# Performance work log

Measured on AMD Instinct MI355X. Metric: run time of the kernel, lower is better.

Reference implementation:

```python
import jax, jax.numpy as jnp
import numpy as np
from jax.ops import segment_sum, segment_max

N, E, C, L = 50000, 600000, 128, 4
H = 2 * C  # GENConv MLP hidden = expansion(2) * in_channels
EPS_MSG = 1e-7   # GENConv message eps
EPS_LN = 1e-5    # PyG LayerNorm eps (graph mode)
EPS_GN = 1e-5    # GraphNorm eps
EPS_SM = 1e-16   # PyG softmax denominator eps


def setup_inputs() -> dict:
    key = jax.random.key(0)
    ks = jax.random.split(key, 8)
    s = 0.05
    return dict(
        x=jax.random.normal(ks[0], (N, C), jnp.float32),
        src=jax.random.randint(ks[1], (E,), 0, N),
        dst=jax.random.randint(ks[2], (E,), 0, N),
        W1=jax.random.normal(ks[3], (L, C, H), jnp.float32) * s,
        b1=jnp.zeros((L, H), jnp.float32),
        ln_w=jnp.ones((L, H), jnp.float32),
        ln_b=jnp.zeros((L, H), jnp.float32),
        W2=jax.random.normal(ks[4], (L, H, C), jnp.float32) * s,
        b2=jnp.zeros((L, C), jnp.float32),
        t=jnp.ones((L,), jnp.float32),      # learn_t=True, init t=1.0
        gn_w=jnp.ones((L, C), jnp.float32),
        gn_b=jnp.zeros((L, C), jnp.float32),
        gn_a=jnp.ones((L, C), jnp.float32),  # GraphNorm mean_scale
        lin_w=jax.random.normal(ks[5], (C, 1), jnp.float32) * s,
        lin_b=jnp.zeros((1,), jnp.float32),
    )


def graph_norm(x, w, b, a):
    # single graph: per-channel mean over nodes
    mean = x.mean(axis=0)
    out = x - a * mean
    var = (out * out).mean(axis=0)
    return w * out / jnp.sqrt(var + EPS_GN) + b


def gen_conv(x, src, dst, t, W1, b1, ln_w, ln_b, W2, b2):
    # message: relu(x_j) + eps  (no edge_attr)
    msg = jax.nn.relu(x[src]) + EPS_MSG           # [E, C]
    z = t * msg
    m = segment_max(z, dst, num_segments=N)        # [N, C]
    ex = jnp.exp(z - m[dst])
    den = segment_sum(ex, dst, num_segments=N) + EPS_SM
    alpha = ex / den[dst]                          # per-node per-channel softmax
    agg = segment_sum(msg * alpha, dst, num_segments=N)  # [N, C]
    out = agg + x                                  # root add
    # MLP([C, 2C, C]) with PyG LayerNorm (graph mode) + ReLU between layers
    h = out @ W1 + b1                              # [N, H]
    h = (h - h.mean()) / (h.std() + EPS_LN)        # graph-mode LN: scalar stats
    h = jax.nn.relu(h * ln_w + ln_b)
    return h @ W2 + b2                             # [N, C]


def reference(x, src, dst, W1, b1, ln_w, ln_b, W2, b2, t, gn_w, gn_b, gn_a, lin_w, lin_b):
    for l in range(L):
        # DeepGCNLayer block='res+': norm -> act -> (dropout=0) -> conv, residual add
        h = graph_norm(x, gn_w[l], gn_b[l], gn_a[l])
        h = jax.nn.relu(h)
        h = gen_conv(h, src, dst, t[l], W1[l], b1[l], ln_w[l], ln_b[l], W2[l], b2[l])
        x = x + h
    return x @ lin_w + lin_b                       # [N, 1]
```

## Files before the change

kernel.cpp:

```cpp
#include <hip/hip_runtime.h>

#define C_DIM 128
#define H_DIM 256
#define L_NUM 4

typedef __attribute__((ext_vector_type(8))) short bf16x8;
typedef __attribute__((ext_vector_type(4))) float f32x4;

__device__ __forceinline__ unsigned short f2bf(float f){
  unsigned u = __builtin_bit_cast(unsigned, f);
  u = u + 0x7FFFu + ((u >> 16) & 1u);
  return (unsigned short)(u >> 16);
}
__device__ __forceinline__ float bf2f(unsigned short b){
  return __builtin_bit_cast(float, ((unsigned)b) << 16);
}

__global__ void k_hist(const int* __restrict__ dst, int* __restrict__ cnt, int E){
  for (int e = blockIdx.x*blockDim.x + threadIdx.x; e < E; e += gridDim.x*blockDim.x)
    atomicAdd(cnt + dst[e], 1);
}

__global__ void k_scan_local(const int* __restrict__ cnt, int* __restrict__ rp,
                             int* __restrict__ bsum, int N){
  __shared__ int tmp[256];
  int t = threadIdx.x; int i = blockIdx.x*256 + t;
  int v = (i < N) ? cnt[i] : 0;
  tmp[t] = v; __syncthreads();
  for (int off = 1; off < 256; off <<= 1){
    int x = (t >= off) ? tmp[t-off] : 0; __syncthreads();
    tmp[t] += x; __syncthreads();
  }
  if (i < N) rp[i] = tmp[t] - v;
  if (t == 255) bsum[blockIdx.x] = tmp[t];
}

__global__ void k_scan_bsums(const int* __restrict__ bsum, int* __restrict__ boff, int nb){
  __shared__ int tmp[256];
  int t = threadIdx.x;
  int v = (t < nb) ? bsum[t] : 0;
  tmp[t] = v; __syncthreads();
  for (int off = 1; off < 256; off <<= 1){
    int x = (t >= off) ? tmp[t-off] : 0; __syncthreads();
    tmp[t] += x; __syncthreads();
  }
  if (t < nb) boff[t] = tmp[t] - v;
}

__global__ void k_scan_add(int* __restrict__ rp, const int* __restrict__ boff, int N, int E){
  int i = blockIdx.x*256 + threadIdx.x;
  if (i < N) rp[i] += boff[blockIdx.x];
  if (i == 0) rp[N] = E;
}

__global__ void k_scatter(const int* __restrict__ src, const int* __restrict__ dst,
                          const int* __restrict__ rp, int* __restrict__ cnt,
                          int* __restrict__ csrc, int E){
  for (int e = blockIdx.x*blockDim.x + threadIdx.x; e < E; e += gridDim.x*blockDim.x){
    int d = dst[e];
    int pos = rp[d] + atomicAdd(cnt + d, 1);
    csrc[pos] = src[e];
  }
}

__global__ void k_wconv(const float* __restrict__ W1, const float* __restrict__ W2,
                        unsigned short* __restrict__ W1t, unsigned short* __restrict__ W2t){
  int i = blockIdx.x*blockDim.x + threadIdx.x;
  if (i >= L_NUM*C_DIM*H_DIM) return;
  int l = i >> 15, r = i & 32767;
  { int k = r >> 8, n = r & 255;  W1t[l*32768 + n*128 + k] = f2bf(W1[i]); }
  { int k = r >> 7, n = r & 127;  W2t[l*32768 + n*256 + k] = f2bf(W2[i]); }
}

__global__ void k_stat0(const float* __restrict__ X, float* __restrict__ part, int NB, int N){
  int t = threadIdx.x; int c = t & 127; int half = t >> 7;
  int r0 = blockIdx.x*128, rend = min(r0 + 128, N);
  float s = 0.f, s2 = 0.f;
  for (int r = r0 + half; r < rend; r += 2){
    float v = X[r*C_DIM + c]; s += v; s2 += v*v;
  }
  __shared__ float a1[256], a2[256];
  a1[t] = s; a2[t] = s2; __syncthreads();
  if (t < 128){
    part[t*NB + blockIdx.x]       = a1[t] + a1[t+128];
    part[(128+t)*NB + blockIdx.x] = a2[t] + a2[t+128];
  }
}

__global__ void k_gn_coef(const float* __restrict__ part, int NB, int nb,
                          const float* __restrict__ gw, const float* __restrict__ gb,
                          const float* __restrict__ ga, float* __restrict__ coef, int N){
  int c = blockIdx.x;
  int t = threadIdx.x;
  float s = 0.f, s2 = 0.f;
  for (int i = t; i < nb; i += 256){
    s  += part[c*NB + i];
    s2 += part[(128+c)*NB + i];
  }
  __shared__ float sh1[256], sh2[256];
  sh1[t] = s; sh2[t] = s2; __syncthreads();
  for (int off = 128; off; off >>= 1){
    if (t < off){ sh1[t] += sh1[t+off]; sh2[t] += sh2[t+off]; }
    __syncthreads();
  }
  if (t == 0){
    float inv = 1.f/(float)N;
    float mean = sh1[0]*inv;
    float am = ga[c]*mean;
    float var = sh2[0]*inv - 2.f*am*mean + am*am;
    float scale = gw[c] * rsqrtf(var + 1e-5f);
    coef[c] = scale;
    coef[128+c] = gb[c] - scale*am;
  }
}

__global__ void k_gpre(const float* __restrict__ X, const float* __restrict__ coef,
                       unsigned* __restrict__ G2, int total4){
  int i = blockIdx.x*blockDim.x + threadIdx.x;
  if (i >= total4) return;
  int c4 = i & 31;
  float4 x = ((const float4*)X)[i];
  float4 A = ((const float4*)coef)[c4];
  float4 B = ((const float4*)coef)[32 + c4];
  float o0 = fmaxf(A.x*x.x + B.x, 0.f);
  float o1 = fmaxf(A.y*x.y + B.y, 0.f);
  float o2 = fmaxf(A.z*x.z + B.z, 0.f);
  float o3 = fmaxf(A.w*x.w + B.w, 0.f);
  uint2 pk = make_uint2((unsigned)f2bf(o0) | ((unsigned)f2bf(o1) << 16),
                        (unsigned)f2bf(o2) | ((unsigned)f2bf(o3) << 16));
  ((uint2*)G2)[i] = pk;
}

__global__ void k_agg(const unsigned* __restrict__ G, const int* __restrict__ rp,
                      const int* __restrict__ csrc, const float* __restrict__ tptr, int l,
                      unsigned short* __restrict__ U, int N){
  int wave = threadIdx.x >> 6, lane = threadIdx.x & 63;
  int n = blockIdx.x*4 + wave;
  if (n >= N) return;
  float tv = tptr[l];
  int jb = rp[n], je = rp[n+1];
  float d0 = 0.f, d1 = 0.f, s0 = 0.f, s1 = 0.f;

  #define EDGE(uu) { \
    float msg0 = bf2f((unsigned short)((uu) & 0xffff)) + 1e-7f; \
    float msg1 = bf2f((unsigned short)((uu) >> 16)) + 1e-7f; \
    float e0 = __expf(fminf(tv*msg0, 60.f)); \
    float e1 = __expf(fminf(tv*msg1, 60.f)); \
    d0 += e0; d1 += e1; s0 += msg0*e0; s1 += msg1*e1; }

  int j = jb;
  for (; j + 3 < je; j += 4){
    int i0 = csrc[j], i1 = csrc[j+1], i2 = csrc[j+2], i3 = csrc[j+3];
    unsigned u0 = G[i0*64 + lane];
    unsigned u1 = G[i1*64 + lane];
    unsigned u2 = G[i2*64 + lane];
    unsigned u3 = G[i3*64 + lane];
    EDGE(u0); EDGE(u1); EDGE(u2); EDGE(u3);
  }
  for (; j < je; ++j){
    unsigned u = G[csrc[j]*64 + lane];
    EDGE(u);
  }
  #undef EDGE

  unsigned uo = G[n*64 + lane];
  float g0 = bf2f((unsigned short)(uo & 0xffff));
  float g1 = bf2f((unsigned short)(uo >> 16));
  float u0 = s0/(d0 + 1e-16f) + g0;
  float u1 = s1/(d1 + 1e-16f) + g1;
  unsigned pk = (unsigned)f2bf(u0) | ((unsigned)f2bf(u1) << 16);
  *(unsigned*)(U + n*C_DIM + lane*2) = pk;
}

__global__ void k_gemm1(const unsigned short* __restrict__ A, const unsigned short* __restrict__ Bt,
                        const float* __restrict__ b1, unsigned short* __restrict__ H1,
                        float* __restrict__ part, int M){
  __shared__ __align__(16) char smem[64*256];
  __shared__ float rbuf[8];
  const int tid = threadIdx.x;
  const int m0 = blockIdx.x * 64;
  const int wave = tid >> 6, lane = tid & 63;
  const int lr = lane & 15, lc = lane >> 4;

  bf16x8 bf[4][4];
  #pragma unroll
  for (int nf = 0; nf < 4; ++nf){
    int n = wave*64 + nf*16 + lr;
    #pragma unroll
    for (int ks = 0; ks < 4; ++ks)
      bf[nf][ks] = *(const bf16x8*)(Bt + n*128 + ks*32 + lc*8);
  }
  #pragma unroll
  for (int p = 0; p < 4; ++p){
    int idx = p*256 + tid;
    int row = idx >> 4, ch = idx & 15;
    int r = m0 + row;
    uint4 v = make_uint4(0u,0u,0u,0u);
    if (r < M) v = *(const uint4*)(A + r*128 + ch*8);
    int o = (row*256 + ch*16) ^ ((row & 7) << 4);
    *(uint4*)(smem + o) = v;
  }
  __syncthreads();

  f32x4 acc[4][4] = {};
  #pragma unroll
  for (int ks = 0; ks < 4; ++ks){
    bf16x8 a[4];
    #pragma unroll
    for (int mf = 0; mf < 4; ++mf){
      int row = mf*16 + lr;
      int o = (row*256 + ks*64 + lc*16) ^ ((row & 7) << 4);
      a[mf] = *(const bf16x8*)(smem + o);
    }
    #pragma unroll
    for (int mf = 0; mf < 4; ++mf)
      #pragma unroll
      for (int nf = 0; nf < 4; ++nf)
        acc[mf][nf] = __builtin_amdgcn_mfma_f32_16x16x32_bf16(a[mf], bf[nf][ks], acc[mf][nf], 0, 0, 0);
  }

  float s1 = 0.f, s2 = 0.f;
  #pragma unroll
  for (int mf = 0; mf < 4; ++mf){
    #pragma unroll
    for (int j = 0; j < 4; ++j){
      int r = m0 + mf*16 + lc*4 + j;
      if (r < M){
        #pragma unroll
        for (int nf = 0; nf < 4; ++nf){
          int col = wave*64 + nf*16 + lr;
          float v = acc[mf][nf][j] + b1[col];
          H1[r*H_DIM + col] = f2bf(v);
          s1 += v; s2 += v*v;
        }
      }
    }
  }
  #pragma unroll
  for (int o = 32; o; o >>= 1){ s1 += __shfl_down(s1, o); s2 += __shfl_down(s2, o); }
  if (lane == 0){ rbuf[wave] = s1; rbuf[4 + wave] = s2; }
  __syncthreads();
  if (tid == 0)
    part[blockIdx.x*2]     = rbuf[0]+rbuf[1]+rbuf[2]+rbuf[3];
  if (tid == 1)
    part[blockIdx.x*2 + 1] = rbuf[4]+rbuf[5]+rbuf[6]+rbuf[7];
}

__global__ void k_ln_coef(const float* __restrict__ part, int nb,
                          const float* __restrict__ lnw, const float* __restrict__ lnb,
                          float* __restrict__ coef, int M){
  __shared__ float s1s[256], s2s[256];
  int t = threadIdx.x;
  float s1 = 0.f, s2 = 0.f;
  for (int i = t; i < nb; i += 256){ s1 += part[2*i]; s2 += part[2*i+1]; }
  s1s[t] = s1; s2s[t] = s2; __syncthreads();
  for (int off = 128; off; off >>= 1){
    if (t < off){ s1s[t] += s1s[t+off]; s2s[t] += s2s[t+off]; }
    __syncthreads();
  }
  double NH = (double)M * (double)H_DIM;
  double mean = (double)s1s[0] / NH;
  double var = (double)s2s[0] / NH - mean*mean;
  double sd = sqrt(var > 0.0 ? var : 0.0);
  float denom = (float)sd + 1e-5f;
  float wv = lnw[t] / denom;
  coef[t] = wv;
  coef[256 + t] = lnb[t] - (float)mean * wv;
}

__global__ void k_gemm2(const unsigned short* __restrict__ H1, const float* __restrict__ lncoef,
                        const unsigned short* __restrict__ Bt, const float* __restrict__ b2,
                        float* __restrict__ X, float* __restrict__ part, int NB, int M){
  __shared__ __align__(16) char smem[64*512];
  const int tid = threadIdx.x;
  const int m0 = blockIdx.x * 64;
  const int wave = tid >> 6, lane = tid & 63;
  const int lr = lane & 15, lc = lane >> 4;
  const float* colw = lncoef;
  const float* colb = lncoef + 256;

  bf16x8 bf[2][8];
  #pragma unroll
  for (int nf = 0; nf < 2; ++nf){
    int n = wave*32 + nf*16 + lr;
    #pragma unroll
    for (int ks = 0; ks < 8; ++ks)
      bf[nf][ks] = *(const bf16x8*)(Bt + n*256 + ks*32 + lc*8);
  }
  #pragma unroll
  for (int p = 0; p < 8; ++p){
    int idx = (p*256 + tid)*8;
    int row = idx >> 8, col = idx & 255;
    int r = m0 + row;
    uint4 v = make_uint4(0u,0u,0u,0u);
    if (r < M) v = *(const uint4*)(H1 + r*H_DIM + col);
    unsigned short hb[8] = {(unsigned short)(v.x&0xffff),(unsigned short)(v.x>>16),
                            (unsigned short)(v.y&0xffff),(unsigned short)(v.y>>16),
                            (unsigned short)(v.z&0xffff),(unsigned short)(v.z>>16),
                            (unsigned short)(v.w&0xffff),(unsigned short)(v.w>>16)};
    unsigned outp[4];
    #pragma unroll
    for (int q = 0; q < 4; ++q){
      float f0 = fmaxf(colw[col+2*q]  *bf2f(hb[2*q])   + colb[col+2*q],   0.f);
      float f1 = fmaxf(colw[col+2*q+1]*bf2f(hb[2*q+1]) + colb[col+2*q+1], 0.f);
      outp[q] = (unsigned)f2bf(f0) | ((unsigned)f2bf(f1) << 16);
    }
    int o = (row*512 + col*2) ^ ((row & 7) << 4);
    *(uint4*)(smem + o) = make_uint4(outp[0],outp[1],outp[2],outp[3]);
  }
  __syncthreads();

  f32x4 acc[4][2] = {};
  #pragma unroll
  for (int ks = 0; ks < 8; ++ks){
    bf16x8 a[4];
    #pragma unroll
    for (int mf = 0; mf < 4; ++mf){
      int row = mf*16 + lr;
      int o = (row*512 + ks*64 + lc*16) ^ ((row & 7) << 4);
      a[mf] = *(const bf16x8*)(smem + o);
    }
    #pragma unroll
    for (int mf = 0; mf < 4; ++mf)
      #pragma unroll
      for (int nf = 0; nf < 2; ++nf)
        acc[mf][nf] = __builtin_amdgcn_mfma_f32_16x16x32_bf16(a[mf], bf[nf][ks], acc[mf][nf], 0, 0, 0);
  }

  float sA[2] = {0.f, 0.f}, sB[2] = {0.f, 0.f};
  #pragma unroll
  for (int mf = 0; mf < 4; ++mf){
    #pragma unroll
    for (int j = 0; j < 4; ++j){
      int r = m0 + mf*16 + lc*4 + j;
      if (r < M){
        #pragma unroll
        for (int nf = 0; nf < 2; ++nf){
          int col = wave*32 + nf*16 + lr;
          float v = X[r*C_DIM + col] + acc[mf][nf][j] + b2[col];
          X[r*C_DIM + col] = v;
          sA[nf] += v; sB[nf] += v*v;
        }
      }
    }
  }
  #pragma unroll
  for (int nf = 0; nf < 2; ++nf){
    sA[nf] += __shfl_xor(sA[nf], 16); sA[nf] += __shfl_xor(sA[nf], 32);
    sB[nf] += __shfl_xor(sB[nf], 16); sB[nf] += __shfl_xor(sB[nf], 32);
  }
  if (lane < 16){
    #pragma unroll
    for (int nf = 0; nf < 2; ++nf){
      int col = wave*32 + nf*16 + lr;
      part[col*NB + blockIdx.x]       = sA[nf];
      part[(128+col)*NB + blockIdx.x] = sB[nf];
    }
  }
}

__global__ void k_final(const float* __restrict__ X, const float* __restrict__ lw,
                        const float* __restrict__ lb, float* __restrict__ out, int N){
  int wave = threadIdx.x >> 6, lane = threadIdx.x & 63;
  int n = blockIdx.x*4 + wave;
  if (n >= N) return;
  float2 v = *(const float2*)(X + n*C_DIM + lane*2);
  float2 w = *(const float2*)(lw + lane*2);
  float s = v.x*w.x + v.y*w.y;
  #pragma unroll
  for (int o = 32; o; o >>= 1) s += __shfl_down(s, o);
  if (lane == 0) out[n] = s + lb[0];
}

extern "C" void kernel_launch(void* const* d_in, const int* in_sizes, int n_in,
                              void* d_out, int out_size, void* d_ws, size_t ws_size,
                              hipStream_t stream){
  const float* x    = (const float*)d_in[0];
  const int*   src  = (const int*)d_in[1];
  const int*   dst  = (const int*)d_in[2];
  const float* W1   = (const float*)d_in[3];
  const float* b1   = (const float*)d_in[4];
  const float* lnw  = (const float*)d_in[5];
  const float* lnb  = (const float*)d_in[6];
  const float* W2   = (const float*)d_in[7];
  const float* b2   = (const float*)d_in[8];
  const float* tpt  = (const float*)d_in[9];
  const float* gnw  = (const float*)d_in[10];
  const float* gnb  = (const float*)d_in[11];
  const float* gna  = (const float*)d_in[12];
  const float* linw = (const float*)d_in[13];
  const float* linb = (const float*)d_in[14];
  (void)n_in; (void)out_size; (void)ws_size;
  const int N = in_sizes[0] / C_DIM;
  const int E = in_sizes[1];
  float* out = (float*)d_out;

  const int gmw = (N + 63)/64;
  const int S0  = (N + 127)/128;
  const int NB  = gmw;

  char* wsp = (char*)d_ws; size_t off = 0;
  auto alloc = [&](size_t b)->char*{ char* p = wsp + off; off += (b + 255) & ~(size_t)255; return p; };
  int* cnt          = (int*)alloc((size_t)N*4);
  int* rp           = (int*)alloc((size_t)(N+1)*4);
  int* bsum         = (int*)alloc(1024);
  int* boff         = (int*)alloc(1024);
  float* gncoef     = (float*)alloc(1024);
  float* lncoef     = (float*)alloc(2048);
  float* lnpart     = (float*)alloc((size_t)gmw*2*4);
  float* part       = (float*)alloc((size_t)NB*256*4);
  int* csrc         = (int*)alloc((size_t)E*4);
  unsigned short* W1t = (unsigned short*)alloc((size_t)L_NUM*C_DIM*H_DIM*2);
  unsigned short* W2t = (unsigned short*)alloc((size_t)L_NUM*C_DIM*H_DIM*2);
  unsigned* g       = (unsigned*)alloc((size_t)N*C_DIM*2);
  unsigned short* U = (unsigned short*)alloc((size_t)N*C_DIM*2);
  unsigned short* h1 = (unsigned short*)alloc((size_t)N*H_DIM*2);
  float* xc         = (float*)alloc((size_t)N*C_DIM*4);

  const int SB = (N + 255)/256;
  hipMemsetAsync(cnt, 0, (size_t)N*4, stream);
  k_hist<<<1024, 256, 0, stream>>>(dst, cnt, E);
  k_scan_local<<<SB, 256, 0, stream>>>(cnt, rp, bsum, N);
  k_scan_bsums<<<1, 256, 0, stream>>>(bsum, boff, SB);
  k_scan_add<<<SB, 256, 0, stream>>>(rp, boff, N, E);
  hipMemsetAsync(cnt, 0, (size_t)N*4, stream);
  k_scatter<<<1024, 256, 0, stream>>>(src, dst, rp, cnt, csrc, E);
  k_wconv<<<(L_NUM*C_DIM*H_DIM + 255)/256, 256, 0, stream>>>(W1, W2, W1t, W2t);
  hipMemcpyAsync(xc, x, (size_t)N*C_DIM*4, hipMemcpyDeviceToDevice, stream);
  k_stat0<<<S0, 256, 0, stream>>>(x, part, NB, N);

  for (int l = 0; l < L_NUM; ++l){
    int nb = (l == 0) ? S0 : gmw;
    k_gn_coef<<<128, 256, 0, stream>>>(part, NB, nb, gnw + l*C_DIM, gnb + l*C_DIM, gna + l*C_DIM, gncoef, N);
    k_gpre<<<(N*32 + 255)/256, 256, 0, stream>>>(xc, gncoef, g, N*32);
    k_agg<<<(N + 3)/4, 256, 0, stream>>>(g, rp, csrc, tpt, l, U, N);
    k_gemm1<<<gmw, 256, 0, stream>>>(U, W1t + (size_t)l*C_DIM*H_DIM, b1 + l*H_DIM, h1, lnpart, N);
    k_ln_coef<<<1, 256, 0, stream>>>(lnpart, gmw, lnw + l*H_DIM, lnb + l*H_DIM, lncoef, N);
    k_gemm2<<<gmw, 256, 0, stream>>>(h1, lncoef, W2t + (size_t)l*C_DIM*H_DIM, b2 + l*C_DIM, xc, part, NB, N);
  }
  k_final<<<(N + 3)/4, 256, 0, stream>>>(xc, linw, linb, out, N);
}
```

Baseline: 479.2 us.

## Fuse LN-coef, final projection into gemm2; shuffle-broadcast CSR indices in agg

The aggregation kernel now loads up to 64 neighbour indices per wave in one coalesced read and broadcasts them with shuffles, instead of every lane reading each index. The LayerNorm coefficient reduction is folded into the prologue of every gemm2 block, which removes one single-block launch per layer but makes each block redundantly reduce the partials. The final linear projection is fused into the last layer's gemm2, which then skips writing X. The initial device copy of x is dropped by reading x directly in layer 0.

```diff
diff --git a/kernel.cpp b/kernel.cpp
--- a/kernel.cpp
+++ b/kernel.cpp
@@ -148,18 +148,25 @@
     float e1 = __expf(fminf(tv*msg1, 60.f)); \
     d0 += e0; d1 += e1; s0 += msg0*e0; s1 += msg1*e1; }
 
-  int j = jb;
-  for (; j + 3 < je; j += 4){
-    int i0 = csrc[j], i1 = csrc[j+1], i2 = csrc[j+2], i3 = csrc[j+3];
-    unsigned u0 = G[i0*64 + lane];
-    unsigned u1 = G[i1*64 + lane];
-    unsigned u2 = G[i2*64 + lane];
-    unsigned u3 = G[i3*64 + lane];
-    EDGE(u0); EDGE(u1); EDGE(u2); EDGE(u3);
-  }
-  for (; j < je; ++j){
-    unsigned u = G[csrc[j]*64 + lane];
-    EDGE(u);
+  for (int base = jb; base < je; base += 64){
+    int cnt = min(64, je - base);
+    int myidx = (base + lane < je) ? csrc[base + lane] : 0;
+    int jj = 0;
+    for (; jj + 3 < cnt; jj += 4){
+      int i0 = __shfl(myidx, jj);
+      int i1 = __shfl(myidx, jj+1);
+      int i2 = __shfl(myidx, jj+2);
+      int i3 = __shfl(myidx, jj+3);
+      unsigned u0 = G[i0*64 + lane];
+      unsigned u1 = G[i1*64 + lane];
+      unsigned u2 = G[i2*64 + lane];
+      unsigned u3 = G[i3*64 + lane];
+      EDGE(u0); EDGE(u1); EDGE(u2); EDGE(u3);
+    }
+    for (; jj < cnt; ++jj){
+      unsigned u = G[__shfl(myidx, jj)*64 + lane];
+      EDGE(u);
+    }
   }
   #undef EDGE
 
@@ -246,38 +253,43 @@
     part[blockIdx.x*2 + 1] = rbuf[4]+rbuf[5]+rbuf[6]+rbuf[7];
 }
 
-__global__ void k_ln_coef(const float* __restrict__ part, int nb,
-                          const float* __restrict__ lnw, const float* __restrict__ lnb,
-                          float* __restrict__ coef, int M){
-  __shared__ float s1s[256], s2s[256];
-  int t = threadIdx.x;
-  float s1 = 0.f, s2 = 0.f;
-  for (int i = t; i < nb; i += 256){ s1 += part[2*i]; s2 += part[2*i+1]; }
-  s1s[t] = s1; s2s[t] = s2; __syncthreads();
-  for (int off = 128; off; off >>= 1){
-    if (t < off){ s1s[t] += s1s[t+off]; s2s[t] += s2s[t+off]; }
-    __syncthreads();
-  }
-  double NH = (double)M * (double)H_DIM;
-  double mean = (double)s1s[0] / NH;
-  double var = (double)s2s[0] / NH - mean*mean;
-  double sd = sqrt(var > 0.0 ? var : 0.0);
-  float denom = (float)sd + 1e-5f;
-  float wv = lnw[t] / denom;
-  coef[t] = wv;
-  coef[256 + t] = lnb[t] - (float)mean * wv;
-}
-
-__global__ void k_gemm2(const unsigned short* __restrict__ H1, const float* __restrict__ lncoef,
+__global__ void k_gemm2(const unsigned short* __restrict__ H1,
+                        const float* __restrict__ lnpart, int nparts,
+                        const float* __restrict__ lnw, const float* __restrict__ lnb,
                         const unsigned short* __restrict__ Bt, const float* __restrict__ b2,
-                        float* __restrict__ X, float* __restrict__ part, int NB, int M){
+                        const float* __restrict__ Xin, float* __restrict__ Xout,
+                        float* __restrict__ part, int NB,
+                        const float* __restrict__ lw, const float* __restrict__ lb,
+                        float* __restrict__ out, int M){
   __shared__ __align__(16) char smem[64*512];
+  __shared__ float red1[256], red2[256];
+  __shared__ float colw[256], colb[256];
+  __shared__ float rowdot[64];
   const int tid = threadIdx.x;
   const int m0 = blockIdx.x * 64;
   const int wave = tid >> 6, lane = tid & 63;
   const int lr = lane & 15, lc = lane >> 4;
-  const float* colw = lncoef;
-  const float* colb = lncoef + 256;
+  const bool last = (lw != nullptr);
+
+  {
+    float s1 = 0.f, s2 = 0.f;
+    for (int i = tid; i < nparts; i += 256){ s1 += lnpart[2*i]; s2 += lnpart[2*i+1]; }
+    red1[tid] = s1; red2[tid] = s2; __syncthreads();
+    for (int o = 128; o; o >>= 1){
+      if (tid < o){ red1[tid] += red1[tid+o]; red2[tid] += red2[tid+o]; }
+      __syncthreads();
+    }
+    double NH = (double)M * (double)H_DIM;
+    double mean = (double)red1[0] / NH;
+    double var = (double)red2[0] / NH - mean*mean;
+    double sd = sqrt(var > 0.0 ? var : 0.0);
+    float denom = (float)sd + 1e-5f;
+    float wv = lnw[tid] / denom;
+    colw[tid] = wv;
+    colb[tid] = lnb[tid] - (float)mean * wv;
+    if (tid < 64) rowdot[tid] = 0.f;
+    __syncthreads();
+  }
 
   bf16x8 bf[2][8];
   #pragma unroll
@@ -334,42 +346,44 @@
     for (int j = 0; j < 4; ++j){
       int r = m0 + mf*16 + lc*4 + j;
       if (r < M){
+        float p = 0.f;
         #pragma unroll
         for (int nf = 0; nf < 2; ++nf){
           int col = wave*32 + nf*16 + lr;
-          float v = X[r*C_DIM + col] + acc[mf][nf][j] + b2[col];
-          X[r*C_DIM + col] = v;
-          sA[nf] += v; sB[nf] += v*v;
+          float v = Xin[r*C_DIM + col] + acc[mf][nf][j] + b2[col];
+          if (!last){
+            Xout[r*C_DIM + col] = v;
+            sA[nf] += v; sB[nf] += v*v;
+          } else {
+            p += v * lw[col];
+          }
+        }
+        if (last){
+          p += __shfl_xor(p, 1); p += __shfl_xor(p, 2);
+          p += __shfl_xor(p, 4); p += __shfl_xor(p, 8);
+          if (lr == 0) atomicAdd(&rowdot[r - m0], p);
         }
       }
     }
   }
-  #pragma unroll
-  for (int nf = 0; nf < 2; ++nf){
-    sA[nf] += __shfl_xor(sA[nf], 16); sA[nf] += __shfl_xor(sA[nf], 32);
-    sB[nf] += __shfl_xor(sB[nf], 16); sB[nf] += __shfl_xor(sB[nf], 32);
-  }
-  if (lane < 16){
+  if (!last){
     #pragma unroll
     for (int nf = 0; nf < 2; ++nf){
-      int col = wave*32 + nf*16 + lr;
-      part[col*NB + blockIdx.x]       = sA[nf];
-      part[(128+col)*NB + blockIdx.x] = sB[nf];
-    }
-  }
-}
-
-__global__ void k_final(const float* __restrict__ X, const float* __restrict__ lw,
-                        const float* __restrict__ lb, float* __restrict__ out, int N){
-  int wave = threadIdx.x >> 6, lane = threadIdx.x & 63;
-  int n = blockIdx.x*4 + wave;
-  if (n >= N) return;
-  float2 v = *(const float2*)(X + n*C_DIM + lane*2);
-  float2 w = *(const float2*)(lw + lane*2);
-  float s = v.x*w.x + v.y*w.y;
-  #pragma unroll
-  for (int o = 32; o; o >>= 1) s += __shfl_down(s, o);
-  if (lane == 0) out[n] = s + lb[0];
+      sA[nf] += __shfl_xor(sA[nf], 16); sA[nf] += __shfl_xor(sA[nf], 32);
+      sB[nf] += __shfl_xor(sB[nf], 16); sB[nf] += __shfl_xor(sB[nf], 32);
+    }
+    if (lane < 16){
+      #pragma unroll
+      for (int nf = 0; nf < 2; ++nf){
+        int col = wave*32 + nf*16 + lr;
+        part[col*NB + blockIdx.x]       = sA[nf];
+        part[(128+col)*NB + blockIdx.x] = sB[nf];
+      }
+    }
+  } else {
+    __syncthreads();
+    if (tid < 64 && m0 + tid < M) out[m0 + tid] = rowdot[tid] + lb[0];
+  }
 }
 
 extern "C" void kernel_launch(void* const* d_in, const int* in_sizes, int n_in,
@@ -406,7 +420,6 @@
   int* bsum         = (int*)alloc(1024);
   int* boff         = (int*)alloc(1024);
   float* gncoef     = (float*)alloc(1024);
-  float* lncoef     = (float*)alloc(2048);
   float* lnpart     = (float*)alloc((size_t)gmw*2*4);
   float* part       = (float*)alloc((size_t)NB*256*4);
   int* csrc         = (int*)alloc((size_t)E*4);
@@ -426,17 +439,19 @@
   hipMemsetAsync(cnt, 0, (size_t)N*4, stream);
   k_scatter<<<1024, 256, 0, stream>>>(src, dst, rp, cnt, csrc, E);
   k_wconv<<<(L_NUM*C_DIM*H_DIM + 255)/256, 256, 0, stream>>>(W1, W2, W1t, W2t);
-  hipMemcpyAsync(xc, x, (size_t)N*C_DIM*4, hipMemcpyDeviceToDevice, stream);
   k_stat0<<<S0, 256, 0, stream>>>(x, part, NB, N);
 
   for (int l = 0; l < L_NUM; ++l){
     int nb = (l == 0) ? S0 : gmw;
+    const float* Xin = (l == 0) ? x : xc;
+    bool lastL = (l == L_NUM - 1);
     k_gn_coef<<<128, 256, 0, stream>>>(part, NB, nb, gnw + l*C_DIM, gnb + l*C_DIM, gna + l*C_DIM, gncoef, N);
-    k_gpre<<<(N*32 + 255)/256, 256, 0, stream>>>(xc, gncoef, g, N*32);
+    k_gpre<<<(N*32 + 255)/256, 256, 0, stream>>>(Xin, gncoef, g, N*32);
     k_agg<<<(N + 3)/4, 256, 0, stream>>>(g, rp, csrc, tpt, l, U, N);
     k_gemm1<<<gmw, 256, 0, stream>>>(U, W1t + (size_t)l*C_DIM*H_DIM, b1 + l*H_DIM, h1, lnpart, N);
-    k_ln_coef<<<1, 256, 0, stream>>>(lnpart, gmw, lnw + l*H_DIM, lnb + l*H_DIM, lncoef, N);
-    k_gemm2<<<gmw, 256, 0, stream>>>(h1, lncoef, W2t + (size_t)l*C_DIM*H_DIM, b2 + l*C_DIM, xc, part, NB, N);
-  }
-  k_final<<<(N + 3)/4, 256, 0, stream>>>(xc, linw, linb, out, N);
-}
+    k_gemm2<<<gmw, 256, 0, stream>>>(h1, lnpart, gmw, lnw + l*H_DIM, lnb + l*H_DIM,
+                                     W2t + (size_t)l*C_DIM*H_DIM, b2 + l*C_DIM,
+                                     Xin, xc, part, NB,
+                                     lastL ? linw : nullptr, linb, out, N);
+  }
+}
```

Result: faster. 449.9 us (-6.1%).
